# Optimization experiments

Hardware: AMD Instinct MI355X
Metric: run time of the kernel (lower is better)

Reference implementation:

```python
import jax, jax.numpy as jnp
import numpy as np
from jax import lax

B, T, C = 32, 4096, 128
CLAMP_LO, CLAMP_HI = 1e-4, 1.0 - 1e-4
LOGIT_ALPHA0 = 0.0                 # logit(0.5)
LOGIT_BETA0 = float(np.log(0.1 / 0.9))  # logit(0.1)


def setup_inputs() -> dict:
    key = jax.random.key(0)
    x = jax.random.normal(key, (B, T, C), dtype=jnp.float32)
    logit_alpha = jnp.full((C,), LOGIT_ALPHA0, dtype=jnp.float32)
    logit_beta = jnp.full((C,), LOGIT_BETA0, dtype=jnp.float32)
    return {"x": x, "logit_alpha": logit_alpha, "logit_beta": logit_beta}


def reference(x, logit_alpha, logit_beta):
    # Holt level+slope exponential smoothing; output is the level series.
    a = jnp.clip(jax.nn.sigmoid(logit_alpha), CLAMP_LO, CLAMP_HI).astype(x.dtype)  # [C]
    b = jnp.clip(jax.nn.sigmoid(logit_beta), CLAMP_LO, CLAMP_HI).astype(x.dtype)   # [C]

    L0 = x[:, 0, :]                       # [B, C]
    slope0 = jnp.zeros_like(L0)

    def step(carry, xt):
        L_prev, slope = carry
        pred = L_prev + slope
        L = pred + a * (xt - pred)
        slope = slope + b * (L - L_prev - slope)
        return (L, slope), L

    xs = jnp.moveaxis(x[:, 1:, :], 1, 0)  # [T-1, B, C], time-major for scan
    _, Ls = lax.scan(step, (L0, slope0), xs)
    out = jnp.concatenate([L0[:, None, :], jnp.moveaxis(Ls, 0, 1)], axis=1)  # [B, T, C]
    return out
```

## Files before the change

### kernel.cpp

```cpp
#include <hip/hip_runtime.h>
#include <math.h>


#define B_ 32
#define T_ 4096
#define C_ 128
#define K_ 64
#define S_ (T_ / K_)
#define C2 (C_ / 2)
#define NCHUNK (B_ * K_)

__device__ __forceinline__ float sig_clamp(float z) {
    float s = 1.0f / (1.0f + expf(-z));
    return fminf(fmaxf(s, 1.0e-4f), 1.0f - 1.0e-4f);
}

#define STEP(xv0, xv1)                                   \
    {                                                    \
        const float p0 = L0 + sl0;                       \
        const float p1 = L1 + sl1;                       \
        const float g0 = a0 * ((xv0) - p0);              \
        const float g1 = a1 * ((xv1) - p1);              \
        L0 = p0 + g0;  sl0 = fmaf(b0, g0, sl0);          \
        L1 = p1 + g1;  sl1 = fmaf(b1, g1, sl1);          \
    }

__global__ __launch_bounds__(256) void p1_offsets(
        const float* __restrict__ x,
        const float* __restrict__ logit_alpha,
        const float* __restrict__ logit_beta,
        float4* __restrict__ w) {
    const int tid = threadIdx.x & 63;
    const int chunk = blockIdx.x * 4 + (threadIdx.x >> 6);
    const int b = chunk >> 6;
    const int k = chunk & (K_ - 1);

    const float2 la2 = ((const float2*)logit_alpha)[tid];
    const float2 lb2 = ((const float2*)logit_beta)[tid];
    const float a0 = sig_clamp(la2.x), a1 = sig_clamp(la2.y);
    const float b0 = sig_clamp(lb2.x), b1 = sig_clamp(lb2.y);

    const float2* xp = (const float2*)x + ((size_t)b * T_ + (size_t)k * S_) * C2 + tid;

    float L0, sl0 = 0.0f, L1, sl1 = 0.0f;
    int t0;
    if (k == 0) {
        const float2 v = xp[0];
        L0 = v.x; L1 = v.y;
        xp += C2;
        t0 = 1;
    } else {
        L0 = 0.0f; L1 = 0.0f;
        t0 = 0;
    }
    #pragma unroll 8
    for (int t = t0; t < S_; ++t) {
        const float2 xv = *xp;
        xp += C2;
        STEP(xv.x, xv.y);
    }
    w[(size_t)chunk * 64 + tid] = make_float4(L0, sl0, L1, sl1);
}

__global__ __launch_bounds__(256) void p2_emit(
        const float* __restrict__ x,
        const float* __restrict__ logit_alpha,
        const float* __restrict__ logit_beta,
        const float4* __restrict__ w,
        float* __restrict__ out) {
    const int tid = threadIdx.x & 63;
    const int chunk = (NCHUNK - 1) - (blockIdx.x * 4 + (threadIdx.x >> 6));
    const int b = chunk >> 6;
    const int k = chunk & (K_ - 1);

    const float2 la2 = ((const float2*)logit_alpha)[tid];
    const float2 lb2 = ((const float2*)logit_beta)[tid];
    const float a0 = sig_clamp(la2.x), a1 = sig_clamp(la2.y);
    const float b0 = sig_clamp(lb2.x), b1 = sig_clamp(lb2.y);

    const size_t off = ((size_t)b * T_ + (size_t)k * S_) * C2 + tid;
    const float2* xp = (const float2*)x + off;
    float2* op = (float2*)out + off;

    float L0, sl0, L1, sl1;
    int t0;
    if (k == 0) {
        const float2 v = xp[0];
        L0 = v.x; L1 = v.y; sl0 = 0.0f; sl1 = 0.0f;
        op[0] = make_float2(L0, L1);
        xp += C2; op += C2;
        t0 = 1;
    } else {
        float m00_0 = 1.0f - a0, m01_0 = 1.0f - a0;
        float m10_0 = -a0 * b0,  m11_0 = 1.0f - a0 * b0;
        float m00_1 = 1.0f - a1, m01_1 = 1.0f - a1;
        float m10_1 = -a1 * b1,  m11_1 = 1.0f - a1 * b1;
        #pragma unroll
        for (int i = 0; i < 6; ++i) {
            float n00 = m00_0 * m00_0 + m01_0 * m10_0;
            float n01 = m00_0 * m01_0 + m01_0 * m11_0;
            float n10 = m10_0 * m00_0 + m11_0 * m10_0;
            float n11 = m10_0 * m01_0 + m11_0 * m11_0;
            m00_0 = n00; m01_0 = n01; m10_0 = n10; m11_0 = n11;
            n00 = m00_1 * m00_1 + m01_1 * m10_1;
            n01 = m00_1 * m01_1 + m01_1 * m11_1;
            n10 = m10_1 * m00_1 + m11_1 * m10_1;
            n11 = m10_1 * m01_1 + m11_1 * m11_1;
            m00_1 = n00; m01_1 = n01; m10_1 = n10; m11_1 = n11;
        }
        const float4* wp = w + (size_t)b * K_ * 64 + tid;
        float4 s = wp[0];
        #pragma unroll 4
        for (int j = 1; j < k; ++j) {
            const float4 wj = wp[(size_t)j * 64];
            const float nx = m00_0 * s.x + m01_0 * s.y + wj.x;
            const float ny = m10_0 * s.x + m11_0 * s.y + wj.y;
            const float nz = m00_1 * s.z + m01_1 * s.w + wj.z;
            const float nw = m10_1 * s.z + m11_1 * s.w + wj.w;
            s = make_float4(nx, ny, nz, nw);
        }
        L0 = s.x; sl0 = s.y; L1 = s.z; sl1 = s.w;
        t0 = 0;
    }

    #pragma unroll 8
    for (int t = t0; t < S_; ++t) {
        const float2 xv = *xp;
        xp += C2;
        STEP(xv.x, xv.y);
        *op = make_float2(L0, L1);
        op += C2;
    }
}

__global__ void seq_fallback(
        const float* __restrict__ x,
        const float* __restrict__ logit_alpha,
        const float* __restrict__ logit_beta,
        float* __restrict__ out) {
    const int tid = blockIdx.x * blockDim.x + threadIdx.x;
    if (tid >= B_ * C_) return;
    const int b = tid / C_;
    const int c = tid % C_;
    const float a0 = sig_clamp(logit_alpha[c]);
    const float b0 = sig_clamp(logit_beta[c]);
    const float* xp = x + (size_t)b * T_ * C_ + c;
    float* op = out + (size_t)b * T_ * C_ + c;
    float L0 = xp[0], sl0 = 0.0f;
    op[0] = L0;
    for (int t = 1; t < T_; ++t) {
        const float xv = xp[(size_t)t * C_];
        const float p0 = L0 + sl0;
        const float g0 = a0 * (xv - p0);
        L0 = p0 + g0;
        sl0 = fmaf(b0, g0, sl0);
        op[(size_t)t * C_] = L0;
    }
}

extern "C" void kernel_launch(void* const* d_in, const int* in_sizes, int n_in,
                              void* d_out, int out_size, void* d_ws, size_t ws_size,
                              hipStream_t stream) {
    const float* x  = (const float*)d_in[0];
    const float* la = (const float*)d_in[1];
    const float* lb = (const float*)d_in[2];
    float* out = (float*)d_out;

    const size_t need = (size_t)NCHUNK * 64 * sizeof(float4);

    if (ws_size >= need) {
        float4* w = (float4*)d_ws;
        p1_offsets<<<NCHUNK / 4, 256, 0, stream>>>(x, la, lb, w);
        p2_emit<<<NCHUNK / 4, 256, 0, stream>>>(x, la, lb, w, out);
    } else {
        seq_fallback<<<(B_ * C_ + 255) / 256, 256, 0, stream>>>(x, la, lb, out);
    }
}
```

Before: 130.4 us.

## Fuse two-pass chunked scan into one cooperative kernel with grid sync

Merges the chunk-aggregate pass and the emit pass into a single cooperative kernel, one 64-thread block per chunk, separated by a grid-wide barrier. The aim is to drop the second kernel launch and to keep x warm in cache between the two passes. In exchange it needs all 2048 blocks co-resident, depends on the grid-sync cost, and runs small 64-thread blocks. If the cooperative launch fails, nothing is computed.

```diff
diff --git a/kernel.cpp b/kernel.cpp
--- a/kernel.cpp
+++ b/kernel.cpp
@@ -1,5 +1,8 @@
 #include <hip/hip_runtime.h>
+#include <hip/hip_cooperative_groups.h>
 #include <math.h>
+
+namespace cg = cooperative_groups;
 
 
 #define B_ 32
@@ -25,71 +28,58 @@
         L1 = p1 + g1;  sl1 = fmaf(b1, g1, sl1);          \
     }
 
-__global__ __launch_bounds__(256) void p1_offsets(
+__global__ __launch_bounds__(64, 4) void coop_scan(
         const float* __restrict__ x,
         const float* __restrict__ logit_alpha,
         const float* __restrict__ logit_beta,
-        float4* __restrict__ w) {
-    const int tid = threadIdx.x & 63;
-    const int chunk = blockIdx.x * 4 + (threadIdx.x >> 6);
+        float4* __restrict__ aggW,
+        float* __restrict__ out) {
+    const int lane = threadIdx.x;
+    const int chunk = blockIdx.x;
     const int b = chunk >> 6;
     const int k = chunk & (K_ - 1);
 
-    const float2 la2 = ((const float2*)logit_alpha)[tid];
-    const float2 lb2 = ((const float2*)logit_beta)[tid];
+    const float2 la2 = ((const float2*)logit_alpha)[lane];
+    const float2 lb2 = ((const float2*)logit_beta)[lane];
     const float a0 = sig_clamp(la2.x), a1 = sig_clamp(la2.y);
     const float b0 = sig_clamp(lb2.x), b1 = sig_clamp(lb2.y);
 
-    const float2* xp = (const float2*)x + ((size_t)b * T_ + (size_t)k * S_) * C2 + tid;
+    const size_t off = ((size_t)b * T_ + (size_t)k * S_) * C2 + lane;
+    const float2* xp = (const float2*)x + off;
 
     float L0, sl0 = 0.0f, L1, sl1 = 0.0f;
-    int t0;
     if (k == 0) {
         const float2 v = xp[0];
         L0 = v.x; L1 = v.y;
-        xp += C2;
-        t0 = 1;
+        #pragma unroll 8
+        for (int t = 1; t < S_; ++t) {
+            const float2 xv = xp[(size_t)t * C2];
+            STEP(xv.x, xv.y);
+        }
     } else {
         L0 = 0.0f; L1 = 0.0f;
-        t0 = 0;
+        #pragma unroll 8
+        for (int t = 0; t < S_; ++t) {
+            const float2 xv = xp[(size_t)t * C2];
+            STEP(xv.x, xv.y);
+        }
     }
-    #pragma unroll 8
-    for (int t = t0; t < S_; ++t) {
-        const float2 xv = *xp;
-        xp += C2;
-        STEP(xv.x, xv.y);
-    }
-    w[(size_t)chunk * 64 + tid] = make_float4(L0, sl0, L1, sl1);
-}
+    aggW[(size_t)chunk * 64 + lane] = make_float4(L0, sl0, L1, sl1);
 
-__global__ __launch_bounds__(256) void p2_emit(
-        const float* __restrict__ x,
-        const float* __restrict__ logit_alpha,
-        const float* __restrict__ logit_beta,
-        const float4* __restrict__ w,
-        float* __restrict__ out) {
-    const int tid = threadIdx.x & 63;
-    const int chunk = (NCHUNK - 1) - (blockIdx.x * 4 + (threadIdx.x >> 6));
-    const int b = chunk >> 6;
-    const int k = chunk & (K_ - 1);
+    __threadfence();
+    cg::this_grid().sync();
 
-    const float2 la2 = ((const float2*)logit_alpha)[tid];
-    const float2 lb2 = ((const float2*)logit_beta)[tid];
-    const float a0 = sig_clamp(la2.x), a1 = sig_clamp(la2.y);
-    const float b0 = sig_clamp(lb2.x), b1 = sig_clamp(lb2.y);
-
-    const size_t off = ((size_t)b * T_ + (size_t)k * S_) * C2 + tid;
-    const float2* xp = (const float2*)x + off;
     float2* op = (float2*)out + off;
-
-    float L0, sl0, L1, sl1;
-    int t0;
     if (k == 0) {
         const float2 v = xp[0];
         L0 = v.x; L1 = v.y; sl0 = 0.0f; sl1 = 0.0f;
         op[0] = make_float2(L0, L1);
-        xp += C2; op += C2;
-        t0 = 1;
+        #pragma unroll 8
+        for (int t = 1; t < S_; ++t) {
+            const float2 xv = xp[(size_t)t * C2];
+            STEP(xv.x, xv.y);
+            op[(size_t)t * C2] = make_float2(L0, L1);
+        }
     } else {
         float m00_0 = 1.0f - a0, m01_0 = 1.0f - a0;
         float m10_0 = -a0 * b0,  m11_0 = 1.0f - a0 * b0;
@@ -108,7 +98,7 @@
             n11 = m10_1 * m01_1 + m11_1 * m11_1;
             m00_1 = n00; m01_1 = n01; m10_1 = n10; m11_1 = n11;
         }
-        const float4* wp = w + (size_t)b * K_ * 64 + tid;
+        const float4* wp = aggW + (size_t)(chunk - k) * 64 + lane;
         float4 s = wp[0];
         #pragma unroll 4
         for (int j = 1; j < k; ++j) {
@@ -120,16 +110,12 @@
             s = make_float4(nx, ny, nz, nw);
         }
         L0 = s.x; sl0 = s.y; L1 = s.z; sl1 = s.w;
-        t0 = 0;
-    }
-
-    #pragma unroll 8
-    for (int t = t0; t < S_; ++t) {
-        const float2 xv = *xp;
-        xp += C2;
-        STEP(xv.x, xv.y);
-        *op = make_float2(L0, L1);
-        op += C2;
+        #pragma unroll 8
+        for (int t = 0; t < S_; ++t) {
+            const float2 xv = xp[(size_t)t * C2];
+            STEP(xv.x, xv.y);
+            op[(size_t)t * C2] = make_float2(L0, L1);
+        }
     }
 }
 
@@ -169,9 +155,11 @@
     const size_t need = (size_t)NCHUNK * 64 * sizeof(float4);
 
     if (ws_size >= need) {
-        float4* w = (float4*)d_ws;
-        p1_offsets<<<NCHUNK / 4, 256, 0, stream>>>(x, la, lb, w);
-        p2_emit<<<NCHUNK / 4, 256, 0, stream>>>(x, la, lb, w, out);
+        float4* aggW = (float4*)d_ws;
+        void* args[] = { (void*)&x, (void*)&la, (void*)&lb,
+                         (void*)&aggW, (void*)&out };
+        hipLaunchCooperativeKernel((const void*)coop_scan,
+                                   dim3(NCHUNK), dim3(64), args, 0, stream);
     } else {
         seq_fallback<<<(B_ * C_ + 255) / 256, 256, 0, stream>>>(x, la, lb, out);
     }
```

Result: slower. 314.4 us (+141.1%).
